# Performance work log

Measured on AMD Instinct MI355X. Metric: run time of the kernel, lower is better.

The kernel has to match this reference:

```python
import jax, jax.numpy as jnp
import numpy as np

LR = 0.01            # learning_rate
PC = 0.001           # pred_clipping
WC = 5.0             # weight_clipping
_LO = float(np.log(PC / (1.0 - PC)))   # logit(pred_clipping)
_HI = -_LO                              # logit(1 - pred_clipping)


def setup_inputs() -> dict:
    B, S, I, CTX, M, C = 64, 1023, 1024, 784, 4, 1  # S = size-1 (bias row), C = num_classes->1
    key = jax.random.key(0)
    k = jax.random.split(key, 6)
    logit = jax.random.normal(k[0], (B, I, C), jnp.float32)
    context = jax.random.normal(k[1], (B, CTX), jnp.float32)
    target = jax.random.uniform(k[2], (B, C), dtype=jnp.float32)
    cm = jax.random.normal(k[3], (C, S, M, CTX), jnp.float32)
    cm = cm / jnp.linalg.norm(cm, axis=-1, keepdims=True)          # unit-norm context maps
    cb = jax.random.normal(k[4], (C, S, M, 1), jnp.float32)        # context bias
    weights = jnp.full((C, S, 2 ** M, I), 1.0 / I, jnp.float32)    # per-context weight table
    bias = jax.random.uniform(k[5], (1, 1, C), jnp.float32, _LO, _HI)
    return {"logit": logit, "context": context, "target": target,
            "context_maps": cm, "context_bias": cb, "weights": weights, "bias": bias}


def reference(logit, context, target, context_maps, context_bias, weights, bias):
    C, S, M, _ = context_maps.shape
    B = context.shape[0]
    # halfspace hashing of the context -> per-(class, neuron, sample) weight-table index
    dist = jnp.einsum('csmk,bk->csmb', context_maps, context)      # [C,S,M,B]
    bits = (dist > context_bias).astype(jnp.int32)
    conv = (2 ** jnp.arange(M, dtype=jnp.int32))[:, None]          # [M,1]
    idx = jnp.sum(bits * conv, axis=-2)                            # [C,S,B] in [0, 2^M)
    ci = jnp.arange(C)[:, None, None]
    si = jnp.arange(S)[None, :, None]
    sel = weights[ci, si, idx]                                     # gather -> [C,S,B,I]
    # batched dot product (torch code does full matmul + diagonal; this is the same math)
    out = jnp.clip(jnp.einsum('csbi,bic->csb', sel, logit), _LO, _HI)
    out_bsc = out.transpose(2, 1, 0)                               # [B,S,C]
    # online weight update (target branch): gather-compute-scatter
    diff = jax.nn.sigmoid(out_bsc) - target[:, None, :]            # [B,S,C]
    upd = LR * diff[..., None] * logit.transpose(0, 2, 1)[:, None, :, :]  # [B,S,C,I]
    new_sel = jnp.clip(sel - upd.transpose(2, 1, 0, 3), -WC, WC)   # [C,S,B,I]
    new_weights = weights.at[ci, si, idx].set(new_sel)             # scatter
    # prepend constant bias neuron
    out_logits = jnp.concatenate([jnp.broadcast_to(bias, (B, 1, C)), out_bsc], axis=1)  # [B,S+1,C]
    return out_logits, new_weights
```

## Files before the change

kernel.cpp:

```cpp
#include <hip/hip_runtime.h>
#include <math.h>

typedef unsigned long long u64;

#define S_DIM 1023
#define B_DIM 64
#define I_DIM 1024
#define CTX_DIM 784
#define CTX4 196
#define NWROWS 16
#define NTASK (S_DIM * NWROWS)

#define LR_C 0.01f
#define WC_C 5.0f
#define LO_C (-6.906754778648554f)
#define HI_C ( 6.906754778648554f)

__device__ __forceinline__ float dot4(float4 a, float4 b) {
    return a.x * b.x + a.y * b.y + a.z * b.z + a.w * b.w;
}

__device__ __forceinline__ float4 upd4(float4 w, float4 a, float c) {
    float4 r;
    r.x = fminf(fmaxf(w.x - c * a.x, -WC_C), WC_C);
    r.y = fminf(fmaxf(w.y - c * a.y, -WC_C), WC_C);
    r.z = fminf(fmaxf(w.z - c * a.z, -WC_C), WC_C);
    r.w = fminf(fmaxf(w.w - c * a.w, -WC_C), WC_C);
    return r;
}

__global__ __launch_bounds__(256) void prep_kernel(
    const float* __restrict__ context,
    const float* __restrict__ bias,
    float4* __restrict__ ctxT4,
    float* __restrict__ out_logits)
{
    int g = blockIdx.x * 256 + threadIdx.x;
    int k4 = g >> 6;
    int b  = g & 63;
    ctxT4[g] = *(const float4*)(context + (size_t)b * CTX_DIM + k4 * 4);
    if (g < B_DIM) out_logits[(size_t)g * (S_DIM + 1)] = bias[0];
}

__global__ __launch_bounds__(256) void gln_idx_kernel(
    const float* __restrict__ cm,
    const float* __restrict__ cb,
    const float4* __restrict__ ctxT4,
    u64* __restrict__ mask_g)
{
    __shared__ float red[4][4][64];
    __shared__ int   bits[4][64];
    __shared__ float cb_lds[4];

    const int s = blockIdx.x;
    const int t = threadIdx.x;
    if (t < 4) cb_lds[t] = cb[s * 4 + t];

    const int b = t & 63;
    const int q = __builtin_amdgcn_readfirstlane(t >> 6);
    const float4* cmr = (const float4*)(cm + (size_t)s * 4 * CTX_DIM);

    float a0 = 0.f, a1 = 0.f, a2 = 0.f, a3 = 0.f;
    const int k0 = q * 49;
    #pragma unroll 7
    for (int kk = 0; kk < 49; ++kk) {
        int k4 = k0 + kk;
        float4 c4 = ctxT4[k4 * 64 + b];
        float4 m0 = cmr[k4];
        float4 m1 = cmr[CTX4 + k4];
        float4 m2 = cmr[2 * CTX4 + k4];
        float4 m3 = cmr[3 * CTX4 + k4];
        a0 += dot4(m0, c4);
        a1 += dot4(m1, c4);
        a2 += dot4(m2, c4);
        a3 += dot4(m3, c4);
    }
    red[q][0][b] = a0;
    red[q][1][b] = a1;
    red[q][2][b] = a2;
    red[q][3][b] = a3;
    __syncthreads();

    {
        int m = t >> 6, bb = t & 63;
        float sum = red[0][m][bb] + red[1][m][bb] + red[2][m][bb] + red[3][m][bb];
        bits[m][bb] = (sum > cb_lds[m]) ? 1 : 0;
    }
    __syncthreads();

    if (t < B_DIM) {
        int v = bits[0][t] + 2 * bits[1][t] + 4 * bits[2][t] + 8 * bits[3][t];
        u64 my = 0;
        #pragma unroll
        for (int kk = 0; kk < NWROWS; ++kk) {
            u64 mk = __ballot(v == kk);
            if (t == kk) my = mk;
        }
        if (t < NWROWS) mask_g[s * NWROWS + t] = my;
    }
}

__global__ __launch_bounds__(256, 4) void gln_row3_kernel(
    const float* __restrict__ logit,
    const float* __restrict__ target,
    const float* __restrict__ weights,
    const u64*   __restrict__ mask_g,
    float* __restrict__ out_logits,
    float* __restrict__ new_weights)
{
    const int wv = threadIdx.x >> 6;
    const int ln = threadIdx.x & 63;
    const int task = blockIdx.x * 4 + wv;
    const int s = task >> 4;

    const float4* wr = (const float4*)weights + (size_t)task * 256;
    float4* dst = (float4*)new_weights + (size_t)task * 256;

    float4 w0 = wr[ln], w1 = wr[ln + 64], w2 = wr[ln + 128], w3 = wr[ln + 192];

    u64 m = mask_g[task];
    if (!m) {
        dst[ln]       = w0;
        dst[ln + 64]  = w1;
        dst[ln + 128] = w2;
        dst[ln + 192] = w3;
        return;
    }
    const int last = 63 - __clzll(m);

    while (m) {
        const int b0 = __builtin_ctzll(m); m &= m - 1;
        int b1 = -1;
        if (m) { b1 = __builtin_ctzll(m); m &= m - 1; }

        const float4* lg0 = (const float4*)logit + (size_t)b0 * 256;
        float4 a00 = lg0[ln], a01 = lg0[ln+64], a02 = lg0[ln+128], a03 = lg0[ln+192];
        float4 a10, a11, a12, a13;
        if (b1 >= 0) {
            const float4* lg1 = (const float4*)logit + (size_t)b1 * 256;
            a10 = lg1[ln]; a11 = lg1[ln+64]; a12 = lg1[ln+128]; a13 = lg1[ln+192];
        } else {
            a10 = a00; a11 = a01; a12 = a02; a13 = a03;
        }

        float p0 = dot4(a00,w0) + dot4(a01,w1) + dot4(a02,w2) + dot4(a03,w3);
        float p1 = dot4(a10,w0) + dot4(a11,w1) + dot4(a12,w2) + dot4(a13,w3);

        #pragma unroll
        for (int off = 32; off; off >>= 1) {
            p0 += __shfl_xor(p0, off, 64);
            p1 += __shfl_xor(p1, off, 64);
        }

        {
            float o = fminf(fmaxf(p0, LO_C), HI_C);
            if (ln == 0) out_logits[(size_t)b0 * (S_DIM + 1) + s + 1] = o;
            if (b0 == last) {
                float c = LR_C * (1.0f / (1.0f + expf(-o)) - target[b0]);
                dst[ln]       = upd4(w0, a00, c);
                dst[ln + 64]  = upd4(w1, a01, c);
                dst[ln + 128] = upd4(w2, a02, c);
                dst[ln + 192] = upd4(w3, a03, c);
            }
        }
        if (b1 >= 0) {
            float o = fminf(fmaxf(p1, LO_C), HI_C);
            if (ln == 0) out_logits[(size_t)b1 * (S_DIM + 1) + s + 1] = o;
            if (b1 == last) {
                float c = LR_C * (1.0f / (1.0f + expf(-o)) - target[b1]);
                dst[ln]       = upd4(w0, a10, c);
                dst[ln + 64]  = upd4(w1, a11, c);
                dst[ln + 128] = upd4(w2, a12, c);
                dst[ln + 192] = upd4(w3, a13, c);
            }
        }
    }
}

extern "C" void kernel_launch(void* const* d_in, const int* in_sizes, int n_in,
                              void* d_out, int out_size, void* d_ws, size_t ws_size,
                              hipStream_t stream) {
    const float* logit   = (const float*)d_in[0];
    const float* context = (const float*)d_in[1];
    const float* target  = (const float*)d_in[2];
    const float* cm      = (const float*)d_in[3];
    const float* cb      = (const float*)d_in[4];
    const float* weights = (const float*)d_in[5];
    const float* bias    = (const float*)d_in[6];

    float* out_logits  = (float*)d_out;
    float* new_weights = out_logits + (size_t)B_DIM * (S_DIM + 1);

    char* ws = (char*)d_ws;
    float4* ctxT4 = (float4*)ws;                 ws += (size_t)CTX4 * B_DIM * 16;
    u64*    mask_g  = (u64*)ws;

    prep_kernel<<<CTX4 * B_DIM / 256, 256, 0, stream>>>(context, bias, ctxT4, out_logits);
    gln_idx_kernel<<<S_DIM, 256, 0, stream>>>(cm, cb, ctxT4, mask_g);
    gln_row3_kernel<<<NTASK / 4, 256, 0, stream>>>(logit, target, weights, mask_g,
                                                   out_logits, new_weights);
}
```

Before: 59.57 us.

## Batch four samples per pass, persistent row kernel, two neurons per idx block

```diff
diff --git a/kernel.cpp b/kernel.cpp
--- a/kernel.cpp
+++ b/kernel.cpp
@@ -10,6 +10,8 @@
 #define CTX4 196
 #define NWROWS 16
 #define NTASK (S_DIM * NWROWS)
+#define ROW_BLOCKS 1024
+#define NWAVES (ROW_BLOCKS * 4)
 
 #define LR_C 0.01f
 #define WC_C 5.0f
@@ -42,23 +44,27 @@
     if (g < B_DIM) out_logits[(size_t)g * (S_DIM + 1)] = bias[0];
 }
 
-__global__ __launch_bounds__(256) void gln_idx_kernel(
+__global__ __launch_bounds__(512) void gln_idx_kernel(
     const float* __restrict__ cm,
     const float* __restrict__ cb,
     const float4* __restrict__ ctxT4,
     u64* __restrict__ mask_g)
 {
-    __shared__ float red[4][4][64];
-    __shared__ int   bits[4][64];
-    __shared__ float cb_lds[4];
-
-    const int s = blockIdx.x;
-    const int t = threadIdx.x;
-    if (t < 4) cb_lds[t] = cb[s * 4 + t];
-
-    const int b = t & 63;
-    const int q = __builtin_amdgcn_readfirstlane(t >> 6);
-    const float4* cmr = (const float4*)(cm + (size_t)s * 4 * CTX_DIM);
+    __shared__ float red[2][4][4][64];
+    __shared__ int   bits[2][4][64];
+    __shared__ float cb_lds[2][4];
+
+    const int t  = threadIdx.x;
+    const int sh = t >> 8;
+    const int tt = t & 255;
+    const int s  = blockIdx.x * 2 + sh;
+    const int se = (s < S_DIM) ? s : (S_DIM - 1);
+
+    if (tt < 4) cb_lds[sh][tt] = cb[se * 4 + tt];
+
+    const int b = tt & 63;
+    const int q = __builtin_amdgcn_readfirstlane(tt >> 6);
+    const float4* cmr = (const float4*)(cm + (size_t)se * 4 * CTX_DIM);
 
     float a0 = 0.f, a1 = 0.f, a2 = 0.f, a3 = 0.f;
     const int k0 = q * 49;
@@ -66,59 +72,49 @@
     for (int kk = 0; kk < 49; ++kk) {
         int k4 = k0 + kk;
         float4 c4 = ctxT4[k4 * 64 + b];
-        float4 m0 = cmr[k4];
-        float4 m1 = cmr[CTX4 + k4];
-        float4 m2 = cmr[2 * CTX4 + k4];
-        float4 m3 = cmr[3 * CTX4 + k4];
-        a0 += dot4(m0, c4);
-        a1 += dot4(m1, c4);
-        a2 += dot4(m2, c4);
-        a3 += dot4(m3, c4);
-    }
-    red[q][0][b] = a0;
-    red[q][1][b] = a1;
-    red[q][2][b] = a2;
-    red[q][3][b] = a3;
+        a0 += dot4(cmr[k4], c4);
+        a1 += dot4(cmr[CTX4 + k4], c4);
+        a2 += dot4(cmr[2 * CTX4 + k4], c4);
+        a3 += dot4(cmr[3 * CTX4 + k4], c4);
+    }
+    red[sh][q][0][b] = a0;
+    red[sh][q][1][b] = a1;
+    red[sh][q][2][b] = a2;
+    red[sh][q][3][b] = a3;
     __syncthreads();
 
     {
-        int m = t >> 6, bb = t & 63;
-        float sum = red[0][m][bb] + red[1][m][bb] + red[2][m][bb] + red[3][m][bb];
-        bits[m][bb] = (sum > cb_lds[m]) ? 1 : 0;
+        int m = tt >> 6, bb = tt & 63;
+        float sum = red[sh][0][m][bb] + red[sh][1][m][bb]
+                  + red[sh][2][m][bb] + red[sh][3][m][bb];
+        bits[sh][m][bb] = (sum > cb_lds[sh][m]) ? 1 : 0;
     }
     __syncthreads();
 
-    if (t < B_DIM) {
-        int v = bits[0][t] + 2 * bits[1][t] + 4 * bits[2][t] + 8 * bits[3][t];
+    if (tt < B_DIM) {
+        int v = bits[sh][0][tt] + 2 * bits[sh][1][tt]
+              + 4 * bits[sh][2][tt] + 8 * bits[sh][3][tt];
         u64 my = 0;
         #pragma unroll
         for (int kk = 0; kk < NWROWS; ++kk) {
             u64 mk = __ballot(v == kk);
-            if (t == kk) my = mk;
-        }
-        if (t < NWROWS) mask_g[s * NWROWS + t] = my;
-    }
-}
-
-__global__ __launch_bounds__(256, 4) void gln_row3_kernel(
-    const float* __restrict__ logit,
-    const float* __restrict__ target,
-    const float* __restrict__ weights,
-    const u64*   __restrict__ mask_g,
-    float* __restrict__ out_logits,
-    float* __restrict__ new_weights)
-{
-    const int wv = threadIdx.x >> 6;
-    const int ln = threadIdx.x & 63;
-    const int task = blockIdx.x * 4 + wv;
-    const int s = task >> 4;
-
+            if (tt == kk) my = mk;
+        }
+        if (tt < NWROWS && s < S_DIM) mask_g[s * NWROWS + tt] = my;
+    }
+}
+
+__device__ __forceinline__ void process_task(
+    int task, int ln,
+    const float* __restrict__ logit, const float* __restrict__ target,
+    const float* __restrict__ weights, const u64* __restrict__ mask_g,
+    float* __restrict__ out_logits, float* __restrict__ new_weights)
+{
     const float4* wr = (const float4*)weights + (size_t)task * 256;
+    float4 w0 = wr[ln], w1 = wr[ln + 64], w2 = wr[ln + 128], w3 = wr[ln + 192];
+    u64 m = mask_g[task];
     float4* dst = (float4*)new_weights + (size_t)task * 256;
 
-    float4 w0 = wr[ln], w1 = wr[ln + 64], w2 = wr[ln + 128], w3 = wr[ln + 192];
-
-    u64 m = mask_g[task];
     if (!m) {
         dst[ln]       = w0;
         dst[ln + 64]  = w1;
@@ -126,30 +122,45 @@
         dst[ln + 192] = w3;
         return;
     }
+    const int s = task >> 4;
     const int last = 63 - __clzll(m);
 
     while (m) {
         const int b0 = __builtin_ctzll(m); m &= m - 1;
-        int b1 = -1;
-        if (m) { b1 = __builtin_ctzll(m); m &= m - 1; }
+        int b1 = -1, b2 = -1, b3 = -1;
+        if (m) { b1 = __builtin_ctzll(m); m &= m - 1;
+            if (m) { b2 = __builtin_ctzll(m); m &= m - 1;
+                if (m) { b3 = __builtin_ctzll(m); m &= m - 1; } } }
 
         const float4* lg0 = (const float4*)logit + (size_t)b0 * 256;
         float4 a00 = lg0[ln], a01 = lg0[ln+64], a02 = lg0[ln+128], a03 = lg0[ln+192];
-        float4 a10, a11, a12, a13;
+        float4 a10 = a00, a11 = a01, a12 = a02, a13 = a03;
+        float4 a20 = a00, a21 = a01, a22 = a02, a23 = a03;
+        float4 a30 = a00, a31 = a01, a32 = a02, a33 = a03;
         if (b1 >= 0) {
-            const float4* lg1 = (const float4*)logit + (size_t)b1 * 256;
-            a10 = lg1[ln]; a11 = lg1[ln+64]; a12 = lg1[ln+128]; a13 = lg1[ln+192];
-        } else {
-            a10 = a00; a11 = a01; a12 = a02; a13 = a03;
+            const float4* lg = (const float4*)logit + (size_t)b1 * 256;
+            a10 = lg[ln]; a11 = lg[ln+64]; a12 = lg[ln+128]; a13 = lg[ln+192];
+        }
+        if (b2 >= 0) {
+            const float4* lg = (const float4*)logit + (size_t)b2 * 256;
+            a20 = lg[ln]; a21 = lg[ln+64]; a22 = lg[ln+128]; a23 = lg[ln+192];
+        }
+        if (b3 >= 0) {
+            const float4* lg = (const float4*)logit + (size_t)b3 * 256;
+            a30 = lg[ln]; a31 = lg[ln+64]; a32 = lg[ln+128]; a33 = lg[ln+192];
         }
 
         float p0 = dot4(a00,w0) + dot4(a01,w1) + dot4(a02,w2) + dot4(a03,w3);
         float p1 = dot4(a10,w0) + dot4(a11,w1) + dot4(a12,w2) + dot4(a13,w3);
+        float p2 = dot4(a20,w0) + dot4(a21,w1) + dot4(a22,w2) + dot4(a23,w3);
+        float p3 = dot4(a30,w0) + dot4(a31,w1) + dot4(a32,w2) + dot4(a33,w3);
 
         #pragma unroll
         for (int off = 32; off; off >>= 1) {
             p0 += __shfl_xor(p0, off, 64);
             p1 += __shfl_xor(p1, off, 64);
+            p2 += __shfl_xor(p2, off, 64);
+            p3 += __shfl_xor(p3, off, 64);
         }
 
         {
@@ -174,7 +185,43 @@
                 dst[ln + 192] = upd4(w3, a13, c);
             }
         }
-    }
+        if (b2 >= 0) {
+            float o = fminf(fmaxf(p2, LO_C), HI_C);
+            if (ln == 0) out_logits[(size_t)b2 * (S_DIM + 1) + s + 1] = o;
+            if (b2 == last) {
+                float c = LR_C * (1.0f / (1.0f + expf(-o)) - target[b2]);
+                dst[ln]       = upd4(w0, a20, c);
+                dst[ln + 64]  = upd4(w1, a21, c);
+                dst[ln + 128] = upd4(w2, a22, c);
+                dst[ln + 192] = upd4(w3, a23, c);
+            }
+        }
+        if (b3 >= 0) {
+            float o = fminf(fmaxf(p3, LO_C), HI_C);
+            if (ln == 0) out_logits[(size_t)b3 * (S_DIM + 1) + s + 1] = o;
+            if (b3 == last) {
+                float c = LR_C * (1.0f / (1.0f + expf(-o)) - target[b3]);
+                dst[ln]       = upd4(w0, a30, c);
+                dst[ln + 64]  = upd4(w1, a31, c);
+                dst[ln + 128] = upd4(w2, a32, c);
+                dst[ln + 192] = upd4(w3, a33, c);
+            }
+        }
+    }
+}
+
+__global__ __launch_bounds__(256, 4) void gln_row4_kernel(
+    const float* __restrict__ logit,
+    const float* __restrict__ target,
+    const float* __restrict__ weights,
+    const u64*   __restrict__ mask_g,
+    float* __restrict__ out_logits,
+    float* __restrict__ new_weights)
+{
+    const int wid = blockIdx.x * 4 + (threadIdx.x >> 6);
+    const int ln  = threadIdx.x & 63;
+    for (int task = wid; task < NTASK; task += NWAVES)
+        process_task(task, ln, logit, target, weights, mask_g, out_logits, new_weights);
 }
 
 extern "C" void kernel_launch(void* const* d_in, const int* in_sizes, int n_in,
@@ -196,7 +243,7 @@
     u64*    mask_g  = (u64*)ws;
 
     prep_kernel<<<CTX4 * B_DIM / 256, 256, 0, stream>>>(context, bias, ctxT4, out_logits);
-    gln_idx_kernel<<<S_DIM, 256, 0, stream>>>(cm, cb, ctxT4, mask_g);
-    gln_row3_kernel<<<NTASK / 4, 256, 0, stream>>>(logit, target, weights, mask_g,
-                                                   out_logits, new_weights);
-}
+    gln_idx_kernel<<<(S_DIM + 1) / 2, 512, 0, stream>>>(cm, cb, ctxT4, mask_g);
+    gln_row4_kernel<<<ROW_BLOCKS, 256, 0, stream>>>(logit, target, weights, mask_g,
+                                                    out_logits, new_weights);
+}
```

Result: slower. 80.00 us (+34.3%).

## Process four weight rows per wave with software-prefetched next row

Applied to the files above, without the earlier changes.

```diff
diff --git a/kernel.cpp b/kernel.cpp
--- a/kernel.cpp
+++ b/kernel.cpp
@@ -66,14 +66,10 @@
     for (int kk = 0; kk < 49; ++kk) {
         int k4 = k0 + kk;
         float4 c4 = ctxT4[k4 * 64 + b];
-        float4 m0 = cmr[k4];
-        float4 m1 = cmr[CTX4 + k4];
-        float4 m2 = cmr[2 * CTX4 + k4];
-        float4 m3 = cmr[3 * CTX4 + k4];
-        a0 += dot4(m0, c4);
-        a1 += dot4(m1, c4);
-        a2 += dot4(m2, c4);
-        a3 += dot4(m3, c4);
+        a0 += dot4(cmr[k4], c4);
+        a1 += dot4(cmr[CTX4 + k4], c4);
+        a2 += dot4(cmr[2 * CTX4 + k4], c4);
+        a3 += dot4(cmr[3 * CTX4 + k4], c4);
     }
     red[q][0][b] = a0;
     red[q][1][b] = a1;
@@ -100,25 +96,13 @@
     }
 }
 
-__global__ __launch_bounds__(256, 4) void gln_row3_kernel(
-    const float* __restrict__ logit,
-    const float* __restrict__ target,
-    const float* __restrict__ weights,
-    const u64*   __restrict__ mask_g,
-    float* __restrict__ out_logits,
-    float* __restrict__ new_weights)
-{
-    const int wv = threadIdx.x >> 6;
-    const int ln = threadIdx.x & 63;
-    const int task = blockIdx.x * 4 + wv;
-    const int s = task >> 4;
-
-    const float4* wr = (const float4*)weights + (size_t)task * 256;
+__device__ __forceinline__ void process_task_pl(
+    int task, int ln, u64 m,
+    float4 w0, float4 w1, float4 w2, float4 w3,
+    const float* __restrict__ logit, const float* __restrict__ target,
+    float* __restrict__ out_logits, float* __restrict__ new_weights)
+{
     float4* dst = (float4*)new_weights + (size_t)task * 256;
-
-    float4 w0 = wr[ln], w1 = wr[ln + 64], w2 = wr[ln + 128], w3 = wr[ln + 192];
-
-    u64 m = mask_g[task];
     if (!m) {
         dst[ln]       = w0;
         dst[ln + 64]  = w1;
@@ -126,6 +110,7 @@
         dst[ln + 192] = w3;
         return;
     }
+    const int s = task >> 4;
     const int last = 63 - __clzll(m);
 
     while (m) {
@@ -177,6 +162,53 @@
     }
 }
 
+__global__ __launch_bounds__(256, 4) void gln_row5_kernel(
+    const float* __restrict__ logit,
+    const float* __restrict__ target,
+    const float* __restrict__ weights,
+    const u64*   __restrict__ mask_g,
+    float* __restrict__ out_logits,
+    float* __restrict__ new_weights)
+{
+    const int wv = threadIdx.x >> 6;
+    const int ln = threadIdx.x & 63;
+    const int base = (blockIdx.x * 4 + wv) * 4;
+
+    const u64 mA = mask_g[base + 0];
+    const u64 mB = mask_g[base + 1];
+    const u64 mC = mask_g[base + 2];
+    const u64 mD = mask_g[base + 3];
+
+    const float4* W = (const float4*)weights;
+    float4 c0, c1, c2, c3, n0, n1, n2, n3;
+
+    {
+        const float4* p = W + (size_t)(base + 0) * 256;
+        c0 = p[ln]; c1 = p[ln + 64]; c2 = p[ln + 128]; c3 = p[ln + 192];
+    }
+    {
+        const float4* p = W + (size_t)(base + 1) * 256;
+        n0 = p[ln]; n1 = p[ln + 64]; n2 = p[ln + 128]; n3 = p[ln + 192];
+    }
+    process_task_pl(base + 0, ln, mA, c0, c1, c2, c3, logit, target, out_logits, new_weights);
+
+    c0 = n0; c1 = n1; c2 = n2; c3 = n3;
+    {
+        const float4* p = W + (size_t)(base + 2) * 256;
+        n0 = p[ln]; n1 = p[ln + 64]; n2 = p[ln + 128]; n3 = p[ln + 192];
+    }
+    process_task_pl(base + 1, ln, mB, c0, c1, c2, c3, logit, target, out_logits, new_weights);
+
+    c0 = n0; c1 = n1; c2 = n2; c3 = n3;
+    {
+        const float4* p = W + (size_t)(base + 3) * 256;
+        n0 = p[ln]; n1 = p[ln + 64]; n2 = p[ln + 128]; n3 = p[ln + 192];
+    }
+    process_task_pl(base + 2, ln, mC, c0, c1, c2, c3, logit, target, out_logits, new_weights);
+
+    process_task_pl(base + 3, ln, mD, n0, n1, n2, n3, logit, target, out_logits, new_weights);
+}
+
 extern "C" void kernel_launch(void* const* d_in, const int* in_sizes, int n_in,
                               void* d_out, int out_size, void* d_ws, size_t ws_size,
                               hipStream_t stream) {
@@ -197,6 +229,6 @@
 
     prep_kernel<<<CTX4 * B_DIM / 256, 256, 0, stream>>>(context, bias, ctxT4, out_logits);
     gln_idx_kernel<<<S_DIM, 256, 0, stream>>>(cm, cb, ctxT4, mask_g);
-    gln_row3_kernel<<<NTASK / 4, 256, 0, stream>>>(logit, target, weights, mask_g,
-                                                   out_logits, new_weights);
-}
+    gln_row5_kernel<<<NTASK / 16, 256, 0, stream>>>(logit, target, weights, mask_g,
+                                                    out_logits, new_weights);
+}
```

After: 62.48 us. +4.9%, slower.

## Compute per-neuron dot products with bf16 MFMA over all 16 weight rows

Applied to the files above, without the earlier changes.

```diff
diff --git a/kernel.cpp b/kernel.cpp
--- a/kernel.cpp
+++ b/kernel.cpp
@@ -2,6 +2,8 @@
 #include <math.h>
 
 typedef unsigned long long u64;
+typedef __attribute__((ext_vector_type(8))) short bf16x8;
+typedef __attribute__((ext_vector_type(4))) float f32x4;
 
 #define S_DIM 1023
 #define B_DIM 64
@@ -29,6 +31,12 @@
     return r;
 }
 
+__device__ __forceinline__ short f2bf(float f) {
+    union { float f; unsigned u; } cv; cv.f = f;
+    unsigned r = cv.u + 0x7fffu + ((cv.u >> 16) & 1u);
+    return (short)(r >> 16);
+}
+
 __global__ __launch_bounds__(256) void prep_kernel(
     const float* __restrict__ context,
     const float* __restrict__ bias,
@@ -40,6 +48,23 @@
     int b  = g & 63;
     ctxT4[g] = *(const float4*)(context + (size_t)b * CTX_DIM + k4 * 4);
     if (g < B_DIM) out_logits[(size_t)g * (S_DIM + 1)] = bias[0];
+}
+
+__global__ __launch_bounds__(256) void pack_kernel(
+    const float* __restrict__ logit,
+    short* __restrict__ pack_b)
+{
+    int g = blockIdx.x * 256 + threadIdx.x;
+    int l  = g & 63;
+    int kb = (g >> 6) & 31;
+    int nt = g >> 11;
+    int b  = nt * 16 + (l & 15);
+    int i0 = kb * 32 + (l >> 4) * 8;
+    const float* src = logit + (size_t)b * I_DIM + i0;
+    bf16x8 v;
+    #pragma unroll
+    for (int j = 0; j < 8; ++j) v[j] = f2bf(src[j]);
+    *(bf16x8*)(pack_b + (size_t)g * 8) = v;
 }
 
 __global__ __launch_bounds__(256) void gln_idx_kernel(
@@ -66,14 +91,10 @@
     for (int kk = 0; kk < 49; ++kk) {
         int k4 = k0 + kk;
         float4 c4 = ctxT4[k4 * 64 + b];
-        float4 m0 = cmr[k4];
-        float4 m1 = cmr[CTX4 + k4];
-        float4 m2 = cmr[2 * CTX4 + k4];
-        float4 m3 = cmr[3 * CTX4 + k4];
-        a0 += dot4(m0, c4);
-        a1 += dot4(m1, c4);
-        a2 += dot4(m2, c4);
-        a3 += dot4(m3, c4);
+        a0 += dot4(cmr[k4], c4);
+        a1 += dot4(cmr[CTX4 + k4], c4);
+        a2 += dot4(cmr[2 * CTX4 + k4], c4);
+        a3 += dot4(cmr[3 * CTX4 + k4], c4);
     }
     red[q][0][b] = a0;
     red[q][1][b] = a1;
@@ -100,80 +121,75 @@
     }
 }
 
-__global__ __launch_bounds__(256, 4) void gln_row3_kernel(
+__global__ __launch_bounds__(256, 4) void gln_mfma_kernel(
     const float* __restrict__ logit,
     const float* __restrict__ target,
     const float* __restrict__ weights,
     const u64*   __restrict__ mask_g,
+    const short* __restrict__ pack_b,
     float* __restrict__ out_logits,
     float* __restrict__ new_weights)
 {
-    const int wv = threadIdx.x >> 6;
-    const int ln = threadIdx.x & 63;
-    const int task = blockIdx.x * 4 + wv;
-    const int s = task >> 4;
-
-    const float4* wr = (const float4*)weights + (size_t)task * 256;
-    float4* dst = (float4*)new_weights + (size_t)task * 256;
-
-    float4 w0 = wr[ln], w1 = wr[ln + 64], w2 = wr[ln + 128], w3 = wr[ln + 192];
-
-    u64 m = mask_g[task];
-    if (!m) {
-        dst[ln]       = w0;
-        dst[ln + 64]  = w1;
-        dst[ln + 128] = w2;
-        dst[ln + 192] = w3;
-        return;
-    }
-    const int last = 63 - __clzll(m);
-
-    while (m) {
-        const int b0 = __builtin_ctzll(m); m &= m - 1;
-        int b1 = -1;
-        if (m) { b1 = __builtin_ctzll(m); m &= m - 1; }
-
-        const float4* lg0 = (const float4*)logit + (size_t)b0 * 256;
-        float4 a00 = lg0[ln], a01 = lg0[ln+64], a02 = lg0[ln+128], a03 = lg0[ln+192];
-        float4 a10, a11, a12, a13;
-        if (b1 >= 0) {
-            const float4* lg1 = (const float4*)logit + (size_t)b1 * 256;
-            a10 = lg1[ln]; a11 = lg1[ln+64]; a12 = lg1[ln+128]; a13 = lg1[ln+192];
+    __shared__ u64   mask_lds[NWROWS];
+    __shared__ int   lastb_lds[NWROWS];
+    __shared__ float coef_lds[NWROWS];
+
+    const int s  = blockIdx.x;
+    const int t  = threadIdx.x;
+    const int wv = t >> 6;
+    const int l  = t & 63;
+
+    if (t < NWROWS) {
+        u64 m = mask_g[s * NWROWS + t];
+        mask_lds[t]  = m;
+        lastb_lds[t] = m ? (63 - __clzll(m)) : -1;
+    }
+
+    const float* Abase = weights + (size_t)s * (NWROWS * I_DIM)
+                       + (size_t)(l & 15) * I_DIM + ((l >> 4) * 8);
+    const bf16x8* Bbase = (const bf16x8*)pack_b + (size_t)wv * 32 * 64 + l;
+    f32x4 acc = {0.f, 0.f, 0.f, 0.f};
+    #pragma unroll 4
+    for (int kb = 0; kb < 32; ++kb) {
+        float4 x = *(const float4*)(Abase + kb * 32);
+        float4 y = *(const float4*)(Abase + kb * 32 + 4);
+        bf16x8 af;
+        af[0] = f2bf(x.x); af[1] = f2bf(x.y); af[2] = f2bf(x.z); af[3] = f2bf(x.w);
+        af[4] = f2bf(y.x); af[5] = f2bf(y.y); af[6] = f2bf(y.z); af[7] = f2bf(y.w);
+        bf16x8 bfr = Bbase[(size_t)kb * 64];
+        acc = __builtin_amdgcn_mfma_f32_16x16x32_bf16(af, bfr, acc, 0, 0, 0);
+    }
+
+    __syncthreads();
+
+    const int col = wv * 16 + (l & 15);
+    #pragma unroll
+    for (int j = 0; j < 4; ++j) {
+        int row = (l >> 4) * 4 + j;
+        u64 m = mask_lds[row];
+        if ((m >> col) & 1) {
+            float o = fminf(fmaxf(acc[j], LO_C), HI_C);
+            out_logits[(size_t)col * (S_DIM + 1) + s + 1] = o;
+            if (col == lastb_lds[row])
+                coef_lds[row] = LR_C * (1.0f / (1.0f + expf(-o)) - target[col]);
+        }
+    }
+    __syncthreads();
+
+    const float4* W4 = (const float4*)(weights + (size_t)s * (NWROWS * I_DIM));
+    float4*       D4 = (float4*)(new_weights + (size_t)s * (NWROWS * I_DIM));
+    const float4* L4 = (const float4*)logit;
+    #pragma unroll 8
+    for (int r = 0; r < NWROWS; ++r) {
+        const int lb = lastb_lds[r];
+        float4 w = W4[r * 256 + t];
+        float4 o;
+        if (lb < 0) {
+            o = w;
         } else {
-            a10 = a00; a11 = a01; a12 = a02; a13 = a03;
+            o = upd4(w, L4[lb * 256 + t], coef_lds[r]);
         }
-
-        float p0 = dot4(a00,w0) + dot4(a01,w1) + dot4(a02,w2) + dot4(a03,w3);
-        float p1 = dot4(a10,w0) + dot4(a11,w1) + dot4(a12,w2) + dot4(a13,w3);
-
-        #pragma unroll
-        for (int off = 32; off; off >>= 1) {
-            p0 += __shfl_xor(p0, off, 64);
-            p1 += __shfl_xor(p1, off, 64);
-        }
-
-        {
-            float o = fminf(fmaxf(p0, LO_C), HI_C);
-            if (ln == 0) out_logits[(size_t)b0 * (S_DIM + 1) + s + 1] = o;
-            if (b0 == last) {
-                float c = LR_C * (1.0f / (1.0f + expf(-o)) - target[b0]);
-                dst[ln]       = upd4(w0, a00, c);
-                dst[ln + 64]  = upd4(w1, a01, c);
-                dst[ln + 128] = upd4(w2, a02, c);
-                dst[ln + 192] = upd4(w3, a03, c);
-            }
-        }
-        if (b1 >= 0) {
-            float o = fminf(fmaxf(p1, LO_C), HI_C);
-            if (ln == 0) out_logits[(size_t)b1 * (S_DIM + 1) + s + 1] = o;
-            if (b1 == last) {
-                float c = LR_C * (1.0f / (1.0f + expf(-o)) - target[b1]);
-                dst[ln]       = upd4(w0, a10, c);
-                dst[ln + 64]  = upd4(w1, a11, c);
-                dst[ln + 128] = upd4(w2, a12, c);
-                dst[ln + 192] = upd4(w3, a13, c);
-            }
-        }
+        D4[r * 256 + t] = o;
     }
 }
 
@@ -192,11 +208,13 @@
     float* new_weights = out_logits + (size_t)B_DIM * (S_DIM + 1);
 
     char* ws = (char*)d_ws;
-    float4* ctxT4 = (float4*)ws;                 ws += (size_t)CTX4 * B_DIM * 16;
-    u64*    mask_g  = (u64*)ws;
+    float4* ctxT4  = (float4*)ws;    ws += (size_t)CTX4 * B_DIM * 16;
+    u64*    mask_g = (u64*)ws;       ws += (size_t)NTASK * 8;
+    short*  packb  = (short*)ws;
 
     prep_kernel<<<CTX4 * B_DIM / 256, 256, 0, stream>>>(context, bias, ctxT4, out_logits);
+    pack_kernel<<<32, 256, 0, stream>>>(logit, packb);
     gln_idx_kernel<<<S_DIM, 256, 0, stream>>>(cm, cb, ctxT4, mask_g);
-    gln_row3_kernel<<<NTASK / 4, 256, 0, stream>>>(logit, target, weights, mask_g,
-                                                   out_logits, new_weights);
-}
+    gln_mfma_kernel<<<S_DIM, 256, 0, stream>>>(logit, target, weights, mask_g, packb,
+                                               out_logits, new_weights);
+}
```

Measured after the change: 81.54 us. 1.37x slower.
